# Kernel tuning notes

Measured on AMD Instinct MI355X. Metric: run time of the kernel, lower is better.

## Reference

```python
import jax, jax.numpy as jnp
import numpy as np

FP8_MAX = 448.0  # max finite value of float8_e4m3fn

M, K, N = 16384, 4096, 4096


def setup_inputs() -> dict:
    key = jax.random.key(0)
    kx, kw = jax.random.split(key)
    x = jax.random.normal(kx, (M, K), dtype=jnp.float32)
    w = jax.random.normal(kw, (K, N), dtype=jnp.float32)
    return {"x": x, "w": w}


def _quantize_e4m3(t, scale):
    # fp32 math, clamp to fp8 range, then round-to-nearest via dtype cast
    q = jnp.clip(t * scale, -FP8_MAX, FP8_MAX)
    return q.astype(jnp.float8_e4m3fn)


def reference(x, w):
    # per-tensor absmax scales (matches absmax_atomic_kernel + scale = fp8_max/absmax)
    sx = FP8_MAX / jnp.max(jnp.abs(x))
    sw = FP8_MAX / jnp.max(jnp.abs(w))
    # quantize activation [M,K] and transposed weight [N,K] to fp8 e4m3
    xq = _quantize_e4m3(x, sx)                # [M,K] fp8
    wq_t = _quantize_e4m3(w.T, sw)            # [N,K] fp8 (transpose_quantize kernel)
    # scaled fp8 matmul with fp32 accumulation, dequantize by combined scale
    y = jnp.einsum("mk,nk->mn", xq.astype(jnp.float32), wq_t.astype(jnp.float32))
    return (y / (sx * sw)).astype(x.dtype)
```

## Files before the change

kernel.cpp:

```cpp
#include <hip/hip_runtime.h>

#define FP8_MAX 448.0f

typedef float f32x16 __attribute__((ext_vector_type(16)));
typedef int v8i __attribute__((ext_vector_type(8)));
typedef int v4i __attribute__((ext_vector_type(4)));

__device__ __forceinline__ void load_lds16(const void* g, void* l) {
  __builtin_amdgcn_global_load_lds(
      (__attribute__((address_space(1))) void*)g,
      (__attribute__((address_space(3))) void*)l,
      16, 0, 0);
}

__global__ void init_scales_kernel(unsigned* s) {
  s[0] = 0u;
  s[1] = 0u;
}

__global__ void absmax_kernel(const float4* __restrict__ in,
                              unsigned* __restrict__ out, int n4) {
  float m = 0.f;
  int stride = gridDim.x * blockDim.x;
  for (int i = blockIdx.x * blockDim.x + threadIdx.x; i < n4; i += stride) {
    float4 v = in[i];
    m = fmaxf(m, fmaxf(fmaxf(fabsf(v.x), fabsf(v.y)),
                       fmaxf(fabsf(v.z), fabsf(v.w))));
  }
#pragma unroll
  for (int off = 32; off > 0; off >>= 1)
    m = fmaxf(m, __shfl_down(m, off, 64));
  __shared__ float sred[4];
  int lane = threadIdx.x & 63;
  int wid = threadIdx.x >> 6;
  if (lane == 0) sred[wid] = m;
  __syncthreads();
  if (threadIdx.x == 0) {
    m = fmaxf(fmaxf(sred[0], sred[1]), fmaxf(sred[2], sred[3]));
    atomicMax(out, __float_as_uint(m));
  }
}

__global__ void quant_x_kernel(const float4* __restrict__ x,
                               unsigned* __restrict__ xq,
                               const unsigned* __restrict__ sc, int n4) {
  int t = blockIdx.x * blockDim.x + threadIdx.x;
  if (t >= n4) return;
  float s = FP8_MAX / __uint_as_float(sc[0]);
  float4 v = x[t];
  float q0 = fminf(fmaxf(v.x * s, -FP8_MAX), FP8_MAX);
  float q1 = fminf(fmaxf(v.y * s, -FP8_MAX), FP8_MAX);
  float q2 = fminf(fmaxf(v.z * s, -FP8_MAX), FP8_MAX);
  float q3 = fminf(fmaxf(v.w * s, -FP8_MAX), FP8_MAX);
  int p = __builtin_amdgcn_cvt_pk_fp8_f32(q0, q1, 0, false);
  p = __builtin_amdgcn_cvt_pk_fp8_f32(q2, q3, p, true);
  xq[t] = (unsigned)p;
}

__global__ void quant_wt_kernel(const float* __restrict__ w,
                                unsigned char* __restrict__ wq,
                                const unsigned* __restrict__ sc, int K, int N) {
  __shared__ float tile[64][65];
  float s = FP8_MAX / __uint_as_float(sc[1]);
  int nt = blockIdx.x * 64;
  int kt = blockIdx.y * 64;
#pragma unroll
  for (int it = 0; it < 4; ++it) {
    int idx = threadIdx.x + it * 256;
    int r = idx >> 4;
    int c = (idx & 15) * 4;
    float4 v = *(const float4*)&w[(size_t)(kt + r) * N + nt + c];
    tile[r][c + 0] = v.x; tile[r][c + 1] = v.y;
    tile[r][c + 2] = v.z; tile[r][c + 3] = v.w;
  }
  __syncthreads();
  int n = threadIdx.x >> 2;
  int k0 = (threadIdx.x & 3) * 16;
  unsigned r4[4];
#pragma unroll
  for (int q = 0; q < 4; ++q) {
    float a0 = fminf(fmaxf(tile[k0 + q * 4 + 0][n] * s, -FP8_MAX), FP8_MAX);
    float a1 = fminf(fmaxf(tile[k0 + q * 4 + 1][n] * s, -FP8_MAX), FP8_MAX);
    float a2 = fminf(fmaxf(tile[k0 + q * 4 + 2][n] * s, -FP8_MAX), FP8_MAX);
    float a3 = fminf(fmaxf(tile[k0 + q * 4 + 3][n] * s, -FP8_MAX), FP8_MAX);
    int p = __builtin_amdgcn_cvt_pk_fp8_f32(a0, a1, 0, false);
    p = __builtin_amdgcn_cvt_pk_fp8_f32(a2, a3, p, true);
    r4[q] = (unsigned)p;
  }
  uint4 o;
  o.x = r4[0]; o.y = r4[1]; o.z = r4[2]; o.w = r4[3];
  *(uint4*)&wq[(size_t)(nt + n) * K + kt + k0] = o;
}

__global__ __launch_bounds__(256) void gemm_fp8_kernel(
    const unsigned char* __restrict__ A,
    const unsigned char* __restrict__ B,
    float* __restrict__ C,
    const unsigned* __restrict__ am, int M, int N, int K) {
  __shared__ unsigned char lA[128 * 64];
  __shared__ unsigned char lB[128 * 64];

  const int tid = threadIdx.x;
  const int lane = tid & 63;
  const int wave = tid >> 6;
  const int wm = (wave >> 1) * 64;
  const int wn = (wave & 1) * 64;
  const int l31 = lane & 31;
  const int kh = lane >> 5;

  const int m0 = blockIdx.y * 128;
  const int n0 = blockIdx.x * 128;

  f32x16 acc[2][2];
#pragma unroll
  for (int i = 0; i < 2; ++i)
#pragma unroll
    for (int j = 0; j < 2; ++j)
#pragma unroll
      for (int r = 0; r < 16; ++r) acc[i][j][r] = 0.f;

  const int row0 = tid >> 2;
  const int sc0 = (tid & 3) ^ (row0 & 3);
  const int row1 = row0 + 64;
  const unsigned char* gA0 = A + (size_t)(m0 + row0) * K + sc0 * 16;
  const unsigned char* gA1 = A + (size_t)(m0 + row1) * K + sc0 * 16;
  const unsigned char* gB0 = B + (size_t)(n0 + row0) * K + sc0 * 16;
  const unsigned char* gB1 = B + (size_t)(n0 + row1) * K + sc0 * 16;
  unsigned char* sA0 = &lA[tid * 16];
  unsigned char* sA1 = &lA[(tid + 256) * 16];
  unsigned char* sB0 = &lB[tid * 16];
  unsigned char* sB1 = &lB[(tid + 256) * 16];

  int aoff[2][2], boff[2][2];
#pragma unroll
  for (int sub = 0; sub < 2; ++sub) {
    int ra = wm + sub * 32 + l31;
    int fa = ra & 3;
    aoff[sub][0] = ra * 64 + ((kh * 2 + 0) ^ fa) * 16;
    aoff[sub][1] = ra * 64 + ((kh * 2 + 1) ^ fa) * 16;
    int rb = wn + sub * 32 + l31;
    int fb = rb & 3;
    boff[sub][0] = rb * 64 + ((kh * 2 + 0) ^ fb) * 16;
    boff[sub][1] = rb * 64 + ((kh * 2 + 1) ^ fb) * 16;
  }

  for (int k0 = 0; k0 < K; k0 += 64) {
    load_lds16(gA0 + k0, sA0);
    load_lds16(gA1 + k0, sA1);
    load_lds16(gB0 + k0, sB0);
    load_lds16(gB1 + k0, sB1);
    __syncthreads();

    v8i af[2], bf[2];
#pragma unroll
    for (int sub = 0; sub < 2; ++sub) {
      v4i alo = *(const v4i*)&lA[aoff[sub][0]];
      v4i ahi = *(const v4i*)&lA[aoff[sub][1]];
      af[sub] = __builtin_shufflevector(alo, ahi, 0, 1, 2, 3, 4, 5, 6, 7);
      v4i blo = *(const v4i*)&lB[boff[sub][0]];
      v4i bhi = *(const v4i*)&lB[boff[sub][1]];
      bf[sub] = __builtin_shufflevector(blo, bhi, 0, 1, 2, 3, 4, 5, 6, 7);
    }
#pragma unroll
    for (int si = 0; si < 2; ++si)
#pragma unroll
      for (int sj = 0; sj < 2; ++sj)
        acc[si][sj] = __builtin_amdgcn_mfma_scale_f32_32x32x64_f8f6f4(
            af[si], bf[sj], acc[si][sj],
            0, 0,
            0, 0x7f7f7f7f,
            0, 0x7f7f7f7f);

    __syncthreads();
  }

  float ax = __uint_as_float(am[0]);
  float aw = __uint_as_float(am[1]);
  float sx = FP8_MAX / ax;
  float sw = FP8_MAX / aw;
  float inv = 1.f / (sx * sw);

#pragma unroll
  for (int si = 0; si < 2; ++si)
#pragma unroll
    for (int sj = 0; sj < 2; ++sj) {
      int colbase = n0 + wn + sj * 32 + l31;
#pragma unroll
      for (int r = 0; r < 16; ++r) {
        int row = m0 + wm + si * 32 + (r & 3) + 8 * (r >> 2) + 4 * kh;
        C[(size_t)row * N + colbase] = acc[si][sj][r] * inv;
      }
    }
}

extern "C" void kernel_launch(void* const* d_in, const int* in_sizes, int n_in,
                              void* d_out, int out_size, void* d_ws,
                              size_t ws_size, hipStream_t stream) {
  const int M = 16384, K = 4096, N = 4096;
  const float* x = (const float*)d_in[0];
  const float* w = (const float*)d_in[1];
  float* out = (float*)d_out;

  unsigned* scales = (unsigned*)d_ws;
  unsigned char* xq = (unsigned char*)d_ws + 256;
  unsigned char* wq = xq + (size_t)M * K;

  init_scales_kernel<<<1, 1, 0, stream>>>(scales);
  absmax_kernel<<<8192, 256, 0, stream>>>((const float4*)x, scales + 0,
                                          M * K / 4);
  absmax_kernel<<<2048, 256, 0, stream>>>((const float4*)w, scales + 1,
                                          K * N / 4);
  quant_x_kernel<<<(M * K / 4 + 255) / 256, 256, 0, stream>>>(
      (const float4*)x, (unsigned*)xq, scales, M * K / 4);
  quant_wt_kernel<<<dim3(N / 64, K / 64), 256, 0, stream>>>(w, wq, scales, K,
                                                            N);
  gemm_fp8_kernel<<<dim3(N / 128, M / 128), 256, 0, stream>>>(xq, wq, out,
                                                              scales, M, N, K);
}
```

Before: 925.9 us.

## Rewrite FP8 GEMM with 256x256 tiles, double-buffered LDS and interleaved pipeline

Replaces the simple 128x128 single-buffered GEMM with a 256x256 tile, 512-thread kernel that uses 128KB of double-buffered LDS with 128-wide K steps. Global-to-LDS loads are interleaved with MFMA phases under manual waitcnt, barriers and setprio, and a block-index swizzle is added for L2 locality. The quant_x kernel becomes grid-stride with a fixed grid. This targets the GEMM's exposed memory latency and low data reuse, at the cost of high LDS use, which limits occupancy, and fragile hand-written synchronisation.

```diff
diff --git a/kernel.cpp b/kernel.cpp
--- a/kernel.cpp
+++ b/kernel.cpp
@@ -44,17 +44,18 @@
 __global__ void quant_x_kernel(const float4* __restrict__ x,
                                unsigned* __restrict__ xq,
                                const unsigned* __restrict__ sc, int n4) {
-  int t = blockIdx.x * blockDim.x + threadIdx.x;
-  if (t >= n4) return;
   float s = FP8_MAX / __uint_as_float(sc[0]);
-  float4 v = x[t];
-  float q0 = fminf(fmaxf(v.x * s, -FP8_MAX), FP8_MAX);
-  float q1 = fminf(fmaxf(v.y * s, -FP8_MAX), FP8_MAX);
-  float q2 = fminf(fmaxf(v.z * s, -FP8_MAX), FP8_MAX);
-  float q3 = fminf(fmaxf(v.w * s, -FP8_MAX), FP8_MAX);
-  int p = __builtin_amdgcn_cvt_pk_fp8_f32(q0, q1, 0, false);
-  p = __builtin_amdgcn_cvt_pk_fp8_f32(q2, q3, p, true);
-  xq[t] = (unsigned)p;
+  int stride = gridDim.x * blockDim.x;
+  for (int t = blockIdx.x * blockDim.x + threadIdx.x; t < n4; t += stride) {
+    float4 v = x[t];
+    float q0 = fminf(fmaxf(v.x * s, -FP8_MAX), FP8_MAX);
+    float q1 = fminf(fmaxf(v.y * s, -FP8_MAX), FP8_MAX);
+    float q2 = fminf(fmaxf(v.z * s, -FP8_MAX), FP8_MAX);
+    float q3 = fminf(fmaxf(v.w * s, -FP8_MAX), FP8_MAX);
+    int p = __builtin_amdgcn_cvt_pk_fp8_f32(q0, q1, 0, false);
+    p = __builtin_amdgcn_cvt_pk_fp8_f32(q2, q3, p, true);
+    xq[t] = (unsigned)p;
+  }
 }
 
 __global__ void quant_wt_kernel(const float* __restrict__ w,
@@ -92,105 +93,180 @@
   *(uint4*)&wq[(size_t)(nt + n) * K + kt + k0] = o;
 }
 
-__global__ __launch_bounds__(256) void gemm_fp8_kernel(
+
+#define BAR() asm volatile("s_barrier" ::: "memory")
+#define WAIT_LGKM0()                                        \
+  do {                                                      \
+    asm volatile("s_waitcnt lgkmcnt(0)" ::: "memory");      \
+    __builtin_amdgcn_sched_barrier(0);                      \
+  } while (0)
+#define WAIT_VM(N)                                          \
+  do {                                                      \
+    asm volatile("s_waitcnt vmcnt(" #N ")" ::: "memory");   \
+    __builtin_amdgcn_sched_barrier(0);                      \
+  } while (0)
+
+#define MM(d, a, b)                                              \
+  d = __builtin_amdgcn_mfma_scale_f32_32x32x64_f8f6f4(           \
+      (a), (b), (d), 0, 0, 0, 0x7f7f7f7f, 0, 0x7f7f7f7f)
+
+__device__ __forceinline__ v8i rd_frag(const unsigned char* p, int b0, int b1) {
+  v4i lo = *(const v4i*)(p + b0);
+  v4i hi = *(const v4i*)(p + b1);
+  return __builtin_shufflevector(lo, hi, 0, 1, 2, 3, 4, 5, 6, 7);
+}
+
+#define KTILE(RA, RB, WA, WB, KOFF)                                            \
+  {                                                                            \
+                                                 \
+    af00 = rd_frag((RA) + raB[0], (khx + 0) ^ fxA[0], (khx + 16) ^ fxA[0]);    \
+    af01 = rd_frag((RA) + raB[0], (khx + 64) ^ fxA[0], (khx + 80) ^ fxA[0]);   \
+    af10 = rd_frag((RA) + raB[1], (khx + 0) ^ fxA[1], (khx + 16) ^ fxA[1]);    \
+    af11 = rd_frag((RA) + raB[1], (khx + 64) ^ fxA[1], (khx + 80) ^ fxA[1]);   \
+    bf00 = rd_frag((RB) + qB[0], (khx + 0) ^ fxB, (khx + 16) ^ fxB);           \
+    bf01 = rd_frag((RB) + qB[0], (khx + 64) ^ fxB, (khx + 80) ^ fxB);          \
+    load_lds16(gA0 + 0 * kA + (KOFF), (WA) + 0 * 8192 + ldst);                 \
+    load_lds16(gA0 + 2 * kA + (KOFF), (WA) + 2 * 8192 + ldst);                 \
+    BAR();                                                                     \
+    WAIT_LGKM0();                                                              \
+    __builtin_amdgcn_s_setprio(1);                                             \
+    MM(acc00, af00, bf00); MM(acc10, af10, bf00);                              \
+    MM(acc00, af01, bf01); MM(acc10, af11, bf01);                              \
+    __builtin_amdgcn_s_setprio(0);                                             \
+    WAIT_VM(4);                                                                \
+    BAR();                                                                     \
+                                                 \
+    bf10 = rd_frag((RB) + qB[1], (khx + 0) ^ fxB, (khx + 16) ^ fxB);           \
+    bf11 = rd_frag((RB) + qB[1], (khx + 64) ^ fxB, (khx + 80) ^ fxB);          \
+    load_lds16(gB0 + 0 * kB + (KOFF), (WB) + 0 * 8192 + ldst);                 \
+    load_lds16(gB0 + 1 * kB + (KOFF), (WB) + 1 * 8192 + ldst);                 \
+    BAR();                                                                     \
+    WAIT_LGKM0();                                                              \
+    __builtin_amdgcn_s_setprio(1);                                             \
+    MM(acc01, af00, bf10); MM(acc11, af10, bf10);                              \
+    MM(acc01, af01, bf11); MM(acc11, af11, bf11);                              \
+    __builtin_amdgcn_s_setprio(0);                                             \
+    WAIT_VM(4);                                                                \
+    BAR();                                                                     \
+                                                 \
+    af00 = rd_frag((RA) + raB[2], (khx + 0) ^ fxA[2], (khx + 16) ^ fxA[2]);    \
+    af01 = rd_frag((RA) + raB[2], (khx + 64) ^ fxA[2], (khx + 80) ^ fxA[2]);   \
+    af10 = rd_frag((RA) + raB[3], (khx + 0) ^ fxA[3], (khx + 16) ^ fxA[3]);    \
+    af11 = rd_frag((RA) + raB[3], (khx + 64) ^ fxA[3], (khx + 80) ^ fxA[3]);   \
+    load_lds16(gB0 + 2 * kB + (KOFF), (WB) + 2 * 8192 + ldst);                 \
+    load_lds16(gB0 + 3 * kB + (KOFF), (WB) + 3 * 8192 + ldst);                 \
+    BAR();                                                                     \
+    WAIT_LGKM0();                                                              \
+    __builtin_amdgcn_s_setprio(1);                                             \
+    MM(acc20, af00, bf00); MM(acc30, af10, bf00);                              \
+    MM(acc20, af01, bf01); MM(acc30, af11, bf01);                              \
+    __builtin_amdgcn_s_setprio(0);                                             \
+    BAR();                                                                     \
+                           \
+    load_lds16(gA0 + 1 * kA + (KOFF), (WA) + 1 * 8192 + ldst);                 \
+    load_lds16(gA0 + 3 * kA + (KOFF), (WA) + 3 * 8192 + ldst);                 \
+    BAR();                                                                     \
+    __builtin_amdgcn_s_setprio(1);                                             \
+    MM(acc21, af00, bf10); MM(acc31, af10, bf10);                              \
+    MM(acc21, af01, bf11); MM(acc31, af11, bf11);                              \
+    __builtin_amdgcn_s_setprio(0);                                             \
+    WAIT_VM(4);                                                                \
+    BAR();                                                                     \
+  }
+
+__global__ __launch_bounds__(512, 2) void gemm_fp8_kernel(
     const unsigned char* __restrict__ A,
     const unsigned char* __restrict__ B,
     float* __restrict__ C,
-    const unsigned* __restrict__ am, int M, int N, int K) {
-  __shared__ unsigned char lA[128 * 64];
-  __shared__ unsigned char lB[128 * 64];
-
-  const int tid = threadIdx.x;
-  const int lane = tid & 63;
-  const int wave = tid >> 6;
-  const int wm = (wave >> 1) * 64;
-  const int wn = (wave & 1) * 64;
+    const unsigned* __restrict__ am, int Mi, int Ni, int Ki) {
+  __shared__ __align__(16) unsigned char sm[131072];
+  unsigned char* const smA0 = sm;
+  unsigned char* const smA1 = sm + 32768;
+  unsigned char* const smB0 = sm + 65536;
+  unsigned char* const smB1 = sm + 98304;
+
+  const int t = threadIdx.x;
+  const int lane = t & 63;
+  const int wave = t >> 6;
+  const int wm = wave >> 2;
+  const int wn = wave & 3;
   const int l31 = lane & 31;
   const int kh = lane >> 5;
-
-  const int m0 = blockIdx.y * 128;
-  const int n0 = blockIdx.x * 128;
-
-  f32x16 acc[2][2];
-#pragma unroll
-  for (int i = 0; i < 2; ++i)
-#pragma unroll
-    for (int j = 0; j < 2; ++j)
-#pragma unroll
-      for (int r = 0; r < 16; ++r) acc[i][j][r] = 0.f;
-
-  const int row0 = tid >> 2;
-  const int sc0 = (tid & 3) ^ (row0 & 3);
-  const int row1 = row0 + 64;
-  const unsigned char* gA0 = A + (size_t)(m0 + row0) * K + sc0 * 16;
-  const unsigned char* gA1 = A + (size_t)(m0 + row1) * K + sc0 * 16;
-  const unsigned char* gB0 = B + (size_t)(n0 + row0) * K + sc0 * 16;
-  const unsigned char* gB1 = B + (size_t)(n0 + row1) * K + sc0 * 16;
-  unsigned char* sA0 = &lA[tid * 16];
-  unsigned char* sA1 = &lA[(tid + 256) * 16];
-  unsigned char* sB0 = &lB[tid * 16];
-  unsigned char* sB1 = &lB[(tid + 256) * 16];
-
-  int aoff[2][2], boff[2][2];
-#pragma unroll
-  for (int sub = 0; sub < 2; ++sub) {
-    int ra = wm + sub * 32 + l31;
-    int fa = ra & 3;
-    aoff[sub][0] = ra * 64 + ((kh * 2 + 0) ^ fa) * 16;
-    aoff[sub][1] = ra * 64 + ((kh * 2 + 1) ^ fa) * 16;
-    int rb = wn + sub * 32 + l31;
-    int fb = rb & 3;
-    boff[sub][0] = rb * 64 + ((kh * 2 + 0) ^ fb) * 16;
-    boff[sub][1] = rb * 64 + ((kh * 2 + 1) ^ fb) * 16;
-  }
-
-  for (int k0 = 0; k0 < K; k0 += 64) {
-    load_lds16(gA0 + k0, sA0);
-    load_lds16(gA1 + k0, sA1);
-    load_lds16(gB0 + k0, sB0);
-    load_lds16(gB1 + k0, sB1);
-    __syncthreads();
-
-    v8i af[2], bf[2];
-#pragma unroll
-    for (int sub = 0; sub < 2; ++sub) {
-      v4i alo = *(const v4i*)&lA[aoff[sub][0]];
-      v4i ahi = *(const v4i*)&lA[aoff[sub][1]];
-      af[sub] = __builtin_shufflevector(alo, ahi, 0, 1, 2, 3, 4, 5, 6, 7);
-      v4i blo = *(const v4i*)&lB[boff[sub][0]];
-      v4i bhi = *(const v4i*)&lB[boff[sub][1]];
-      bf[sub] = __builtin_shufflevector(blo, bhi, 0, 1, 2, 3, 4, 5, 6, 7);
-    }
-#pragma unroll
-    for (int si = 0; si < 2; ++si)
-#pragma unroll
-      for (int sj = 0; sj < 2; ++sj)
-        acc[si][sj] = __builtin_amdgcn_mfma_scale_f32_32x32x64_f8f6f4(
-            af[si], bf[sj], acc[si][sj],
-            0, 0,
-            0, 0x7f7f7f7f,
-            0, 0x7f7f7f7f);
-
-    __syncthreads();
-  }
+  const int khx = kh * 32;
+
+  const int bid = blockIdx.y * gridDim.x + blockIdx.x;
+  const int swz = (bid & 7) * 128 + (bid >> 3);
+  const int m0 = (swz >> 4) * 256;
+  const int n0 = (swz & 15) * 256;
+
+  const int rt = t >> 3;
+  const int cst = ((t & 7) ^ (rt & 7)) * 16;
+  const unsigned char* gA0 = A + (size_t)(m0 + rt) * Ki + cst;
+  const unsigned char* gB0 =
+      B + (size_t)(n0 + (rt >> 4) * 64 + (rt & 15)) * Ki + cst;
+  const size_t kA = (size_t)Ki * 64;
+  const size_t kB = (size_t)Ki * 16;
+  const int ldst = t * 16;
+
+  int raB[4], fxA[4];
+#pragma unroll
+  for (int mt = 0; mt < 4; ++mt) {
+    int ra = wm * 128 + mt * 32 + l31;
+    raB[mt] = ra * 128;
+    fxA[mt] = (ra & 7) * 16;
+  }
+  const int q = wn * 16 + (l31 & 15);
+  const int fxB = (q & 7) * 16;
+  int qB[2];
+#pragma unroll
+  for (int nt = 0; nt < 2; ++nt)
+    qB[nt] = (nt * 2 + (l31 >> 4)) * 8192 + q * 128;
+
+  f32x16 zero;
+#pragma unroll
+  for (int r = 0; r < 16; ++r) zero[r] = 0.f;
+  f32x16 acc00 = zero, acc01 = zero, acc10 = zero, acc11 = zero;
+  f32x16 acc20 = zero, acc21 = zero, acc30 = zero, acc31 = zero;
+  v8i af00, af01, af10, af11, bf00, bf01, bf10, bf11;
+
+  load_lds16(gA0 + 0 * kA, smA0 + 0 * 8192 + ldst);
+  load_lds16(gA0 + 2 * kA, smA0 + 2 * 8192 + ldst);
+  load_lds16(gB0 + 0 * kB, smB0 + 0 * 8192 + ldst);
+  load_lds16(gB0 + 1 * kB, smB0 + 1 * 8192 + ldst);
+  load_lds16(gB0 + 2 * kB, smB0 + 2 * 8192 + ldst);
+  load_lds16(gB0 + 3 * kB, smB0 + 3 * 8192 + ldst);
+  load_lds16(gA0 + 1 * kA, smA0 + 1 * 8192 + ldst);
+  load_lds16(gA0 + 3 * kA, smA0 + 3 * 8192 + ldst);
+  WAIT_VM(4);
+  BAR();
+
+  const int KT = Ki >> 7;
+  for (int kt = 0; kt < KT; kt += 2) {
+    const size_t ko1 = (size_t)(kt + 1) * 128;
+    const size_t ko2 = (kt + 2 < KT) ? (size_t)(kt + 2) * 128 : 0;
+    KTILE(smA0, smB0, smA1, smB1, ko1);
+    KTILE(smA1, smB1, smA0, smB0, ko2);
+  }
+  asm volatile("s_waitcnt vmcnt(0)" ::: "memory");
 
   float ax = __uint_as_float(am[0]);
   float aw = __uint_as_float(am[1]);
-  float sx = FP8_MAX / ax;
-  float sw = FP8_MAX / aw;
-  float inv = 1.f / (sx * sw);
-
-#pragma unroll
-  for (int si = 0; si < 2; ++si)
-#pragma unroll
-    for (int sj = 0; sj < 2; ++sj) {
-      int colbase = n0 + wn + sj * 32 + l31;
-#pragma unroll
-      for (int r = 0; r < 16; ++r) {
-        int row = m0 + wm + si * 32 + (r & 3) + 8 * (r >> 2) + 4 * kh;
-        C[(size_t)row * N + colbase] = acc[si][sj][r] * inv;
-      }
-    }
+  float sxs = FP8_MAX / ax;
+  float sws = FP8_MAX / aw;
+  float inv = 1.f / (sxs * sws);
+  const int colb = n0 + wn * 64 + l31;
+
+#define STORE(AV, MT, NT)                                                     \
+  _Pragma("unroll") for (int r = 0; r < 16; ++r) {                            \
+    int row = m0 + wm * 128 + (MT) * 32 + (r & 3) + 8 * (r >> 2) + 4 * kh;    \
+    C[(size_t)row * Ni + colb + (NT) * 32] = AV[r] * inv;                     \
+  }
+  STORE(acc00, 0, 0); STORE(acc01, 0, 1);
+  STORE(acc10, 1, 0); STORE(acc11, 1, 1);
+  STORE(acc20, 2, 0); STORE(acc21, 2, 1);
+  STORE(acc30, 3, 0); STORE(acc31, 3, 1);
+#undef STORE
+  (void)Mi;
 }
 
 extern "C" void kernel_launch(void* const* d_in, const int* in_sizes, int n_in,
@@ -210,10 +286,10 @@
                                           M * K / 4);
   absmax_kernel<<<2048, 256, 0, stream>>>((const float4*)w, scales + 1,
                                           K * N / 4);
-  quant_x_kernel<<<(M * K / 4 + 255) / 256, 256, 0, stream>>>(
-      (const float4*)x, (unsigned*)xq, scales, M * K / 4);
+  quant_x_kernel<<<4096, 256, 0, stream>>>((const float4*)x, (unsigned*)xq,
+                                           scales, M * K / 4);
   quant_wt_kernel<<<dim3(N / 64, K / 64), 256, 0, stream>>>(w, wq, scales, K,
                                                             N);
-  gemm_fp8_kernel<<<dim3(N / 128, M / 128), 256, 0, stream>>>(xq, wq, out,
+  gemm_fp8_kernel<<<dim3(N / 256, M / 256), 512, 0, stream>>>(xq, wq, out,
                                                               scales, M, N, K);
 }
```

Measured after the change: 815.8 us. -11.9%, faster.
